# Performance work log

Hardware: AMD Instinct MI355X
Metric: run time of the kernel (lower is better)

## Reference

```python
import jax, jax.numpy as jnp
import numpy as np

SINKHORN_ITERS = 20
SINKHORN_TEMP = 0.2


def log_sinkhorn(log_alpha, n_iters=SINKHORN_ITERS, temperature=SINKHORN_TEMP):
    """Log-domain Sinkhorn normalization over the last two dims."""
    log_alpha = log_alpha / temperature
    for _ in range(n_iters):
        log_alpha = log_alpha - jax.nn.logsumexp(log_alpha, axis=-1, keepdims=True)
        log_alpha = log_alpha - jax.nn.logsumexp(log_alpha, axis=-2, keepdims=True)
    return jnp.exp(log_alpha)


def setup_inputs() -> dict:
    key = jax.random.key(0)
    k_x, k_a, k_w1, k_wv = jax.random.split(key, 4)
    B = 64
    N, K, BASIS = 1024, 64, 8
    # xavier-uniform-like init scales
    a_bound = np.sqrt(6.0 / (N + N))
    w1_bound = np.sqrt(6.0 / (N + BASIS))
    wv_bound = np.sqrt(6.0 / (K + K))
    x = jax.random.normal(k_x, (B, N * K), dtype=jnp.float32)
    A_logits = jax.random.uniform(k_a, (N, N), dtype=jnp.float32, minval=-a_bound, maxval=a_bound)
    W_1 = jax.random.uniform(k_w1, (N, BASIS), dtype=jnp.float32, minval=-w1_bound, maxval=w1_bound)
    W_V = jax.random.uniform(k_wv, (BASIS, K, K), dtype=jnp.float32, minval=-wv_bound, maxval=wv_bound)
    return {"x": x, "A_logits": A_logits, "W_1": W_1, "W_V": W_V}


def reference(x, A_logits, W_1, W_V):
    B = x.shape[0]
    N, K = A_logits.shape[0], W_V.shape[-1]
    # Doubly-stochastic global mixing matrix A: [N, N]
    A = log_sinkhorn(A_logits)
    # Local block logits via basis combination: [N, K, K]
    W_logits = jnp.einsum('tk,kde->tde', W_1, W_V)
    W = log_sinkhorn(W_logits)
    x_reshaped = x.reshape(B, N, K)
    x_local = jnp.einsum('bni,nio->bno', x_reshaped, W)   # per-block KxK mix
    x_global = jnp.einsum('mn,bno->bmo', A, x_local)       # NxN block mix
    return x_global.reshape(B, N * K)
```

## Files before the change

kernel.cpp:

```cpp
#include <hip/hip_runtime.h>
#include <hip/hip_bf16.h>


#define N_DIM 1024
#define INV_T 5.0f
#define NBAR 16

typedef __attribute__((ext_vector_type(8))) short short8;
typedef __attribute__((ext_vector_type(4))) float float4v;

__device__ __forceinline__ float wave_red_sum(float x) {
#define DPP_ADD(C)                                                            \
  {                                                                           \
    int _y = __builtin_amdgcn_update_dpp(0, __float_as_int(x), (C), 0xf, 0xf, \
                                         true);                               \
    x += __int_as_float(_y);                                                  \
  }
  DPP_ADD(0x111);
  DPP_ADD(0x112);
  DPP_ADD(0x114);
  DPP_ADD(0x118);
  DPP_ADD(0x142);
  DPP_ADD(0x143);
#undef DPP_ADD
  return x;
}

__global__ __launch_bounds__(1024) void k_front(
    const float* __restrict__ x, const float* __restrict__ L,
    const float* __restrict__ W1, const float* __restrict__ WV,
    float* __restrict__ E0, __hip_bfloat16* __restrict__ Eh,
    __hip_bfloat16* __restrict__ El, float* __restrict__ P,
    unsigned* __restrict__ ctrl, float* __restrict__ u_g,
    float* __restrict__ v_g, float* __restrict__ XL, int write_bf16) {
  __shared__ __align__(16) float smem[9600];
  const int t = threadIdx.x;
  const int bid = blockIdx.x;
  const int lane = t & 63;
  const int w = t >> 6;

  if (bid < NBAR) {
    float* v_s = smem;
    float* uS = smem + 1024;
    float* red = smem + 1024 + 64;
    const int b = bid;
    const int r0 = b * 64;
    unsigned* flags = ctrl;

    float e[4][16];
#pragma unroll
    for (int j = 0; j < 4; ++j) {
      const int r = r0 + 4 * w + j;
      const float4* Lr = (const float4*)(L + (size_t)r * N_DIM + lane * 16);
#pragma unroll
      for (int q = 0; q < 4; ++q) {
        float4 f = Lr[q];
        e[j][4 * q + 0] = __expf(f.x * INV_T);
        e[j][4 * q + 1] = __expf(f.y * INV_T);
        e[j][4 * q + 2] = __expf(f.z * INV_T);
        e[j][4 * q + 3] = __expf(f.w * INV_T);
      }
      const size_t off = (size_t)r * N_DIM + lane * 16;
      if (write_bf16) {
        __align__(16) ushort hb[16], lb[16];
#pragma unroll
        for (int q = 0; q < 16; ++q) {
          __hip_bfloat16 h = __float2bfloat16(e[j][q]);
          hb[q] = *(ushort*)&h;
          __hip_bfloat16 l2 = __float2bfloat16(e[j][q] - __bfloat162float(h));
          lb[q] = *(ushort*)&l2;
        }
        *(uint4*)&Eh[off] = *(uint4*)&hb[0];
        *(uint4*)&Eh[off + 8] = *(uint4*)&hb[8];
        *(uint4*)&El[off] = *(uint4*)&lb[0];
        *(uint4*)&El[off + 8] = *(uint4*)&lb[8];
      } else {
        float4* Er = (float4*)(E0 + off);
#pragma unroll
        for (int q = 0; q < 4; ++q) {
          float4 g;
          g.x = e[j][4 * q + 0];
          g.y = e[j][4 * q + 1];
          g.z = e[j][4 * q + 2];
          g.w = e[j][4 * q + 3];
          Er[q] = g;
        }
      }
    }
    v_s[t] = 1.0f;
    __syncthreads();

    float u[4];
    for (int it = 0; it < 20; ++it) {
      float vv[16];
#pragma unroll
      for (int q = 0; q < 4; ++q)
        *(float4*)&vv[4 * q] = *(const float4*)&v_s[lane * 16 + 4 * q];
#pragma unroll
      for (int j = 0; j < 4; ++j) {
        float p = 0.f;
#pragma unroll
        for (int k = 0; k < 16; ++k) p += e[j][k] * vv[k];
        p = wave_red_sum(p);
        float ps =
            __int_as_float(__builtin_amdgcn_readlane(__float_as_int(p), 63));
        u[j] = 1.0f / ps;
      }
      float cpl[16];
#pragma unroll
      for (int k = 0; k < 16; ++k)
        cpl[k] = e[0][k] * u[0] + e[1][k] * u[1] + e[2][k] * u[2] +
                 e[3][k] * u[3];
      if (w >= 8) {
#pragma unroll
        for (int q = 0; q < 4; ++q)
          *(float4*)&red[(w - 8) * 1032 + lane * 16 + 4 * q] =
              *(float4*)&cpl[4 * q];
      }
      __syncthreads();
      if (w < 8) {
        float* rr = &red[w * 1032 + lane * 16];
#pragma unroll
        for (int q = 0; q < 4; ++q) {
          float4 rv = *(float4*)&rr[4 * q];
          rv.x += cpl[4 * q + 0];
          rv.y += cpl[4 * q + 1];
          rv.z += cpl[4 * q + 2];
          rv.w += cpl[4 * q + 3];
          *(float4*)&rr[4 * q] = rv;
        }
      }
      __syncthreads();
      float cp = 0.f;
#pragma unroll
      for (int ww = 0; ww < 8; ++ww) cp += red[ww * 1032 + t];
      float* Pw = P + (it & 1) * (NBAR * N_DIM);
      __hip_atomic_store(&Pw[b * N_DIM + t], cp, __ATOMIC_RELAXED,
                         __HIP_MEMORY_SCOPE_AGENT);
      if (it == 19 && lane == 0) {
#pragma unroll
        for (int j = 0; j < 4; ++j) uS[4 * w + j] = u[j];
      }
      __syncthreads();
      if (t == 0)
        __hip_atomic_store(&flags[b], (unsigned)(it + 1), __ATOMIC_RELAXED,
                           __HIP_MEMORY_SCOPE_AGENT);
      if (w == 0 && lane < NBAR) {
        while (__hip_atomic_load(&flags[lane], __ATOMIC_RELAXED,
                                 __HIP_MEMORY_SCOPE_AGENT) <
               (unsigned)(it + 1))
          __builtin_amdgcn_s_sleep(2);
      }
      __syncthreads();
      float s2 = 0.f;
#pragma unroll
      for (int pb = 0; pb < NBAR; ++pb)
        s2 += __hip_atomic_load(&Pw[pb * N_DIM + t], __ATOMIC_RELAXED,
                                __HIP_MEMORY_SCOPE_AGENT);
      v_s[t] = 1.0f / s2;
      __syncthreads();
    }
    if (t < 64) u_g[r0 + t] = uS[t];
    if (b == 0) v_g[t] = v_s[t];
  } else {
    float* uS2 = smem;
    float* ps = smem + 64;
    float* Ws = smem + 64 + 1024;
    float* Xs = smem + 64 + 1024 + 4096;
    const int idx = bid - NBAR;
    const int cnt = (idx < 64) ? 5 : 4;
    const int base_n = (idx < 64) ? idx * 5 : 320 + (idx - 64) * 4;

    for (int s = 0; s < cnt; ++s) {
      const int n = base_n + s;
      float w1[8];
#pragma unroll
      for (int k = 0; k < 8; ++k) w1[k] = W1[n * 8 + k];

      float ew[4];
#pragma unroll
      for (int j = 0; j < 4; ++j) {
        const int f = j * 1024 + t;
        float acc = 0.f;
#pragma unroll
        for (int k = 0; k < 8; ++k) acc += w1[k] * WV[k * 4096 + f];
        ew[j] = __expf(acc * INV_T);
      }

      float vt = 1.0f;
      for (int it = 0; it < 20; ++it) {
#pragma unroll
        for (int j = 0; j < 4; ++j) {
          float pp = wave_red_sum(ew[j] * vt);
          if (lane == 63) uS2[j * 16 + w] = 1.0f / pp;
        }
        float cp = 0.f;
#pragma unroll
        for (int j = 0; j < 4; ++j) cp += ew[j] * uS2[j * 16 + w];
        ps[w * 64 + lane] = cp;
        __syncthreads();
        float sv = 0.f;
#pragma unroll
        for (int ww = 0; ww < 16; ++ww) sv += ps[ww * 64 + lane];
        vt = 1.0f / sv;
        __syncthreads();
      }

#pragma unroll
      for (int j = 0; j < 4; ++j)
        Ws[(j * 16 + w) * 64 + lane] = ew[j] * uS2[j * 16 + w] * vt;
#pragma unroll
      for (int j = 0; j < 4; ++j) {
        const int f = j * 1024 + t;
        Xs[(f >> 6) * 65 + (f & 63)] =
            x[(size_t)(f >> 6) * 65536 + n * 64 + (f & 63)];
      }
      __syncthreads();

      const int bb = t >> 4;
      const int o4 = (t & 15) * 4;
      float4 a4 = {0.f, 0.f, 0.f, 0.f};
#pragma unroll 4
      for (int i = 0; i < 64; ++i) {
        float4 w4 = *(const float4*)&Ws[i * 64 + o4];
        float xv = Xs[bb * 65 + i];
        a4.x += xv * w4.x;
        a4.y += xv * w4.y;
        a4.z += xv * w4.z;
        a4.w += xv * w4.w;
      }
      *(float4*)&XL[(size_t)n * 4096 + bb * 64 + o4] = a4;
      __syncthreads();
    }
  }
}

__global__ __launch_bounds__(256) void k_xt(const float* __restrict__ XL,
                                            const float* __restrict__ v_g,
                                            __hip_bfloat16* __restrict__ XTh,
                                            __hip_bfloat16* __restrict__ XTl) {
  __shared__ float T[64 * 68];
  __shared__ float vsh[64];
  const int t = threadIdx.x;
  const int n0 = blockIdx.x * 64;
  const int c0 = blockIdx.y * 64;
  if (t < 64) vsh[t] = v_g[n0 + t];
  {
    const int r = t >> 4;
    const int c4 = (t & 15) * 4;
#pragma unroll
    for (int p = 0; p < 4; ++p) {
      float4 f =
          *(const float4*)&XL[(size_t)(n0 + r + 16 * p) * 4096 + c0 + c4];
      *(float4*)&T[(r + 16 * p) * 68 + c4] = f;
    }
  }
  __syncthreads();
  const int cl = t >> 2;
  const int nb = (t & 3) * 16;
  __align__(16) __hip_bfloat16 hbuf[16];
  __align__(16) __hip_bfloat16 lbuf[16];
#pragma unroll
  for (int j = 0; j < 16; ++j) {
    float xv = T[(nb + j) * 68 + cl] * vsh[nb + j];
    __hip_bfloat16 h = __float2bfloat16(xv);
    hbuf[j] = h;
    lbuf[j] = __float2bfloat16(xv - __bfloat162float(h));
  }
  const size_t off = (size_t)(c0 + cl) * 1024 + n0 + nb;
  *(uint4*)&XTh[off] = *(uint4*)&hbuf[0];
  *(uint4*)&XTh[off + 8] = *(uint4*)&hbuf[8];
  *(uint4*)&XTl[off] = *(uint4*)&lbuf[0];
  *(uint4*)&XTl[off + 8] = *(uint4*)&lbuf[8];
}

#define LSTR 72
__global__ __launch_bounds__(256) void k_gemm3(
    const ushort* __restrict__ Eh, const ushort* __restrict__ El,
    const ushort* __restrict__ XTh, const ushort* __restrict__ XTl,
    const float* __restrict__ u_g, float* __restrict__ out) {
  __shared__ ushort As[128 * LSTR];
  __shared__ ushort Xs[128 * LSTR];
  __shared__ float ush[128];
  const int t = threadIdx.x;
  const int m0 = blockIdx.x * 128;
  const int c0 = blockIdx.y * 128;
  const int wid = t >> 6, lane = t & 63;
  const int wm = (wid & 1) * 64, wc = (wid >> 1) * 64;
  const int lm = lane & 15, q = lane >> 4;
  const int sr = t >> 1;
  const int sc = (t & 1) * 32;
  if (t < 128) ush[t] = u_g[m0 + t];

  float4v acc[4][4];
#pragma unroll
  for (int i = 0; i < 4; ++i)
#pragma unroll
    for (int j = 0; j < 4; ++j) acc[i][j] = (float4v){0.f, 0.f, 0.f, 0.f};

  for (int seg = 0; seg < 3; ++seg) {
    const ushort* Ag = (seg == 1) ? El : Eh;
    const ushort* Xg = (seg == 2) ? XTl : XTh;
    for (int k0 = 0; k0 < 1024; k0 += 64) {
      __syncthreads();
      const ushort* ag = Ag + (size_t)(m0 + sr) * 1024 + k0 + sc;
      const ushort* xg = Xg + (size_t)(c0 + sr) * 1024 + k0 + sc;
      uint4 a0 = *(const uint4*)(ag);
      uint4 a1 = *(const uint4*)(ag + 8);
      uint4 a2 = *(const uint4*)(ag + 16);
      uint4 a3 = *(const uint4*)(ag + 24);
      uint4 x0 = *(const uint4*)(xg);
      uint4 x1 = *(const uint4*)(xg + 8);
      uint4 x2 = *(const uint4*)(xg + 16);
      uint4 x3 = *(const uint4*)(xg + 24);
      *(uint4*)&As[sr * LSTR + sc] = a0;
      *(uint4*)&As[sr * LSTR + sc + 8] = a1;
      *(uint4*)&As[sr * LSTR + sc + 16] = a2;
      *(uint4*)&As[sr * LSTR + sc + 24] = a3;
      *(uint4*)&Xs[sr * LSTR + sc] = x0;
      *(uint4*)&Xs[sr * LSTR + sc + 8] = x1;
      *(uint4*)&Xs[sr * LSTR + sc + 16] = x2;
      *(uint4*)&Xs[sr * LSTR + sc + 24] = x3;
      __syncthreads();
#pragma unroll
      for (int kk = 0; kk < 2; ++kk) {
        short8 af[4], xf[4];
#pragma unroll
        for (int i = 0; i < 4; ++i)
          af[i] = *(const short8*)&As[(wm + 16 * i + lm) * LSTR + kk * 32 +
                                      q * 8];
#pragma unroll
        for (int j = 0; j < 4; ++j)
          xf[j] = *(const short8*)&Xs[(wc + 16 * j + lm) * LSTR + kk * 32 +
                                      q * 8];
#pragma unroll
        for (int i = 0; i < 4; ++i)
#pragma unroll
          for (int j = 0; j < 4; ++j)
            acc[i][j] = __builtin_amdgcn_mfma_f32_16x16x32_bf16(
                af[i], xf[j], acc[i][j], 0, 0, 0);
      }
    }
  }
#pragma unroll
  for (int i = 0; i < 4; ++i) {
#pragma unroll
    for (int j = 0; j < 4; ++j) {
      const int ml = wm + 16 * i + q * 4;
      const int m = m0 + ml;
      const int c = c0 + wc + 16 * j + lm;
      const int bb = c >> 6, o = c & 63;
      float* dst = out + (size_t)bb * 65536 + (size_t)m * 64 + o;
#pragma unroll
      for (int r = 0; r < 4; ++r) dst[64 * r] = acc[i][j][r] * ush[ml + r];
    }
  }
}

__global__ __launch_bounds__(256) void k_gemm(const float* __restrict__ E0,
                                              const float* __restrict__ XL,
                                              const float* __restrict__ u_g,
                                              const float* __restrict__ v_g,
                                              float* __restrict__ out) {
  __shared__ float Asm[32][132];
  __shared__ float Xsm[32][132];
  const int t = threadIdx.x;
  const int m0 = blockIdx.x * 128;
  const int c0 = blockIdx.y * 128;
  const int my8 = (t >> 4) * 8;
  const int cx8 = (t & 15) * 8;
  const int kk = t & 31;
  const int rr = t >> 5;
  float acc[8][8] = {};

  for (int k0 = 0; k0 < 1024; k0 += 32) {
#pragma unroll
    for (int s = 0; s < 16; ++s)
      Asm[kk][rr + 8 * s] = E0[(size_t)(m0 + rr + 8 * s) * 1024 + k0 + kk];
#pragma unroll
    for (int s = 0; s < 4; ++s) {
      const int krow = k0 + rr + 8 * s;
      float vk = v_g[krow];
      float4 f = *(const float4*)&XL[(size_t)krow * 4096 + c0 + kk * 4];
      f.x *= vk;
      f.y *= vk;
      f.z *= vk;
      f.w *= vk;
      *(float4*)&Xsm[rr + 8 * s][kk * 4] = f;
    }
    __syncthreads();
#pragma unroll
    for (int k = 0; k < 32; ++k) {
      float a[8], xv[8];
      *(float4*)&a[0] = *(const float4*)&Asm[k][my8];
      *(float4*)&a[4] = *(const float4*)&Asm[k][my8 + 4];
      *(float4*)&xv[0] = *(const float4*)&Xsm[k][cx8];
      *(float4*)&xv[4] = *(const float4*)&Xsm[k][cx8 + 4];
#pragma unroll
      for (int i = 0; i < 8; ++i)
#pragma unroll
        for (int j = 0; j < 8; ++j) acc[i][j] += a[i] * xv[j];
    }
    __syncthreads();
  }

#pragma unroll
  for (int i = 0; i < 8; ++i) {
    const int m = m0 + my8 + i;
    const float um = u_g[m];
    const int c = c0 + cx8;
    const int bb = c >> 6, o = c & 63;
    float* dst = out + (size_t)bb * 65536 + (size_t)m * 64 + o;
#pragma unroll
    for (int j = 0; j < 8; ++j) dst[j] = acc[i][j] * um;
  }
}

extern "C" void kernel_launch(void* const* d_in, const int* in_sizes, int n_in,
                              void* d_out, int out_size, void* d_ws,
                              size_t ws_size, hipStream_t stream) {
  (void)in_sizes;
  (void)n_in;
  (void)out_size;
  const float* x = (const float*)d_in[0];
  const float* Alog = (const float*)d_in[1];
  const float* W1 = (const float*)d_in[2];
  const float* WV = (const float*)d_in[3];
  float* out = (float*)d_out;

  char* ws = (char*)d_ws;
  const size_t MB = 1024 * 1024;
  const size_t KB = 1024;
  const bool use_bf16 = ws_size >= (40 * MB + 256 * KB);

  float* E0;
  float* XL;
  float* P;
  float* u_g;
  float* v_g;
  unsigned* ctrl;
  __hip_bfloat16 *Eh = nullptr, *El = nullptr, *XTh = nullptr, *XTl = nullptr;
  if (use_bf16) {
    E0 = (float*)(ws);
    XL = (float*)(ws + 4 * MB);
    Eh = (__hip_bfloat16*)(ws + 20 * MB);
    El = (__hip_bfloat16*)(ws + 22 * MB);
    XTh = (__hip_bfloat16*)(ws + 24 * MB);
    XTl = (__hip_bfloat16*)(ws + 32 * MB);
    P = (float*)(ws + 40 * MB);
    u_g = (float*)(ws + 40 * MB + 128 * KB);
    v_g = (float*)(ws + 40 * MB + 132 * KB);
    ctrl = (unsigned*)(ws + 40 * MB + 136 * KB);
  } else {
    E0 = (float*)(ws);
    XL = (float*)(ws + 4 * MB);
    P = (float*)(ws + 20 * MB);
    u_g = (float*)(ws + 20 * MB + 128 * KB);
    v_g = (float*)(ws + 20 * MB + 132 * KB);
    ctrl = (unsigned*)(ws + 20 * MB + 136 * KB);
  }

  hipMemsetAsync(ctrl, 0, 4096, stream);
  hipLaunchKernelGGL(k_front, dim3(256), dim3(1024), 0, stream, x, Alog, W1,
                     WV, E0, Eh, El, P, ctrl, u_g, v_g, XL, use_bf16 ? 1 : 0);
  if (use_bf16) {
    hipLaunchKernelGGL(k_xt, dim3(16, 64), dim3(256), 0, stream, XL, v_g, XTh,
                       XTl);
    hipLaunchKernelGGL(k_gemm3, dim3(8, 32), dim3(256), 0, stream,
                       (const ushort*)Eh, (const ushort*)El, (const ushort*)XTh,
                       (const ushort*)XTl, u_g, out);
  } else {
    hipLaunchKernelGGL(k_gemm, dim3(8, 32), dim3(256), 0, stream, E0, XL, u_g,
                       v_g, out);
  }
}
```

Before: 275.9 us.

## Replace flag barrier with sentinel polling and add dynamic work queue

The Sinkhorn blocks no longer use a per-iteration flag barrier. Each iteration writes its partial column sums into its own zeroed slice of P, and readers poll those values directly until none is zero. The slices are cleared by an added memset. After finishing the A-Sinkhorn, those blocks join the per-block W work through an atomic ticket queue, replacing the static assignment, to balance load. The element layout of E and of the reduction buffer changes from per-lane contiguous to lane-interleaved. The trade-offs are an extra memset launch, narrower bf16 stores, and reliance on a zero sentinel that assumes no partial sum is exactly zero.

```diff
diff --git a/kernel.cpp b/kernel.cpp
--- a/kernel.cpp
+++ b/kernel.cpp
@@ -45,66 +45,45 @@
     float* red = smem + 1024 + 64;
     const int b = bid;
     const int r0 = b * 64;
-    unsigned* flags = ctrl;
 
     float e[4][16];
 #pragma unroll
     for (int j = 0; j < 4; ++j) {
       const int r = r0 + 4 * w + j;
-      const float4* Lr = (const float4*)(L + (size_t)r * N_DIM + lane * 16);
-#pragma unroll
-      for (int q = 0; q < 4; ++q) {
-        float4 f = Lr[q];
-        e[j][4 * q + 0] = __expf(f.x * INV_T);
-        e[j][4 * q + 1] = __expf(f.y * INV_T);
-        e[j][4 * q + 2] = __expf(f.z * INV_T);
-        e[j][4 * q + 3] = __expf(f.w * INV_T);
-      }
-      const size_t off = (size_t)r * N_DIM + lane * 16;
+      const float* Lr = L + (size_t)r * N_DIM + lane;
+#pragma unroll
+      for (int k = 0; k < 16; ++k) e[j][k] = __expf(Lr[k * 64] * INV_T);
       if (write_bf16) {
-        __align__(16) ushort hb[16], lb[16];
-#pragma unroll
-        for (int q = 0; q < 16; ++q) {
-          __hip_bfloat16 h = __float2bfloat16(e[j][q]);
-          hb[q] = *(ushort*)&h;
-          __hip_bfloat16 l2 = __float2bfloat16(e[j][q] - __bfloat162float(h));
-          lb[q] = *(ushort*)&l2;
+        __hip_bfloat16* EhR = Eh + (size_t)r * N_DIM + lane;
+        __hip_bfloat16* ElR = El + (size_t)r * N_DIM + lane;
+#pragma unroll
+        for (int k = 0; k < 16; ++k) {
+          __hip_bfloat16 h = __float2bfloat16(e[j][k]);
+          EhR[k * 64] = h;
+          ElR[k * 64] = __float2bfloat16(e[j][k] - __bfloat162float(h));
         }
-        *(uint4*)&Eh[off] = *(uint4*)&hb[0];
-        *(uint4*)&Eh[off + 8] = *(uint4*)&hb[8];
-        *(uint4*)&El[off] = *(uint4*)&lb[0];
-        *(uint4*)&El[off + 8] = *(uint4*)&lb[8];
       } else {
-        float4* Er = (float4*)(E0 + off);
-#pragma unroll
-        for (int q = 0; q < 4; ++q) {
-          float4 g;
-          g.x = e[j][4 * q + 0];
-          g.y = e[j][4 * q + 1];
-          g.z = e[j][4 * q + 2];
-          g.w = e[j][4 * q + 3];
-          Er[q] = g;
-        }
+        float* ER = E0 + (size_t)r * N_DIM + lane;
+#pragma unroll
+        for (int k = 0; k < 16; ++k) ER[k * 64] = e[j][k];
       }
     }
     v_s[t] = 1.0f;
     __syncthreads();
 
-    float u[4];
     for (int it = 0; it < 20; ++it) {
       float vv[16];
 #pragma unroll
-      for (int q = 0; q < 4; ++q)
-        *(float4*)&vv[4 * q] = *(const float4*)&v_s[lane * 16 + 4 * q];
+      for (int k = 0; k < 16; ++k) vv[k] = v_s[k * 64 + lane];
+      float u[4];
 #pragma unroll
       for (int j = 0; j < 4; ++j) {
         float p = 0.f;
 #pragma unroll
         for (int k = 0; k < 16; ++k) p += e[j][k] * vv[k];
         p = wave_red_sum(p);
-        float ps =
-            __int_as_float(__builtin_amdgcn_readlane(__float_as_int(p), 63));
-        u[j] = 1.0f / ps;
+        u[j] = 1.0f /
+               __int_as_float(__builtin_amdgcn_readlane(__float_as_int(p), 63));
       }
       float cpl[16];
 #pragma unroll
@@ -113,66 +92,75 @@
                  e[3][k] * u[3];
       if (w >= 8) {
 #pragma unroll
-        for (int q = 0; q < 4; ++q)
-          *(float4*)&red[(w - 8) * 1032 + lane * 16 + 4 * q] =
-              *(float4*)&cpl[4 * q];
+        for (int k = 0; k < 16; ++k)
+          red[(w - 8) * 1028 + k * 64 + lane] = cpl[k];
       }
       __syncthreads();
       if (w < 8) {
-        float* rr = &red[w * 1032 + lane * 16];
-#pragma unroll
-        for (int q = 0; q < 4; ++q) {
-          float4 rv = *(float4*)&rr[4 * q];
-          rv.x += cpl[4 * q + 0];
-          rv.y += cpl[4 * q + 1];
-          rv.z += cpl[4 * q + 2];
-          rv.w += cpl[4 * q + 3];
-          *(float4*)&rr[4 * q] = rv;
-        }
+#pragma unroll
+        for (int k = 0; k < 16; ++k) red[w * 1028 + k * 64 + lane] += cpl[k];
       }
       __syncthreads();
       float cp = 0.f;
 #pragma unroll
-      for (int ww = 0; ww < 8; ++ww) cp += red[ww * 1032 + t];
-      float* Pw = P + (it & 1) * (NBAR * N_DIM);
-      __hip_atomic_store(&Pw[b * N_DIM + t], cp, __ATOMIC_RELAXED,
+      for (int ww = 0; ww < 8; ++ww) cp += red[ww * 1028 + t];
+      float* Pit = P + (size_t)it * (NBAR * N_DIM);
+      __hip_atomic_store(&Pit[b * N_DIM + t], cp, __ATOMIC_RELAXED,
                          __HIP_MEMORY_SCOPE_AGENT);
       if (it == 19 && lane == 0) {
 #pragma unroll
         for (int j = 0; j < 4; ++j) uS[4 * w + j] = u[j];
       }
-      __syncthreads();
-      if (t == 0)
-        __hip_atomic_store(&flags[b], (unsigned)(it + 1), __ATOMIC_RELAXED,
-                           __HIP_MEMORY_SCOPE_AGENT);
-      if (w == 0 && lane < NBAR) {
-        while (__hip_atomic_load(&flags[lane], __ATOMIC_RELAXED,
-                                 __HIP_MEMORY_SCOPE_AGENT) <
-               (unsigned)(it + 1))
-          __builtin_amdgcn_s_sleep(2);
-      }
-      __syncthreads();
+      unsigned vals[NBAR];
+#pragma unroll
+      for (int pb = 0; pb < NBAR; ++pb)
+        vals[pb] = (pb == b)
+                       ? __float_as_uint(cp)
+                       : __hip_atomic_load(
+                             (const unsigned*)&Pit[pb * N_DIM + t],
+                             __ATOMIC_RELAXED, __HIP_MEMORY_SCOPE_AGENT);
+      for (;;) {
+        unsigned miss = 0u;
+#pragma unroll
+        for (int pb = 0; pb < NBAR; ++pb) miss |= (vals[pb] == 0u) ? 1u : 0u;
+        if (miss == 0u) break;
+#pragma unroll
+        for (int pb = 0; pb < NBAR; ++pb)
+          if (vals[pb] == 0u)
+            vals[pb] = __hip_atomic_load(
+                (const unsigned*)&Pit[pb * N_DIM + t], __ATOMIC_RELAXED,
+                __HIP_MEMORY_SCOPE_AGENT);
+      }
       float s2 = 0.f;
 #pragma unroll
-      for (int pb = 0; pb < NBAR; ++pb)
-        s2 += __hip_atomic_load(&Pw[pb * N_DIM + t], __ATOMIC_RELAXED,
-                                __HIP_MEMORY_SCOPE_AGENT);
+      for (int pb = 0; pb < NBAR; ++pb) s2 += __uint_as_float(vals[pb]);
       v_s[t] = 1.0f / s2;
       __syncthreads();
     }
     if (t < 64) u_g[r0 + t] = uS[t];
     if (b == 0) v_g[t] = v_s[t];
-  } else {
+    __syncthreads();
+  }
+
+  {
     float* uS2 = smem;
     float* ps = smem + 64;
     float* Ws = smem + 64 + 1024;
     float* Xs = smem + 64 + 1024 + 4096;
-    const int idx = bid - NBAR;
-    const int cnt = (idx < 64) ? 5 : 4;
-    const int base_n = (idx < 64) ? idx * 5 : 320 + (idx - 64) * 4;
-
-    for (int s = 0; s < cnt; ++s) {
-      const int n = base_n + s;
+    unsigned* nsh = (unsigned*)(smem + 9500);
+    unsigned* ticket = ctrl + 64;
+
+    if (t == 0)
+      nsh[0] = __hip_atomic_fetch_add(ticket, 1u, __ATOMIC_RELAXED,
+                                      __HIP_MEMORY_SCOPE_AGENT);
+    __syncthreads();
+    int slot = 0;
+    for (;;) {
+      const unsigned n = nsh[slot];
+      if (n >= 1024u) break;
+      if (t == 0)
+        nsh[slot ^ 1] = __hip_atomic_fetch_add(ticket, 1u, __ATOMIC_RELAXED,
+                                               __HIP_MEMORY_SCOPE_AGENT);
       float w1[8];
 #pragma unroll
       for (int k = 0; k < 8; ++k) w1[k] = W1[n * 8 + k];
@@ -194,10 +182,10 @@
           float pp = wave_red_sum(ew[j] * vt);
           if (lane == 63) uS2[j * 16 + w] = 1.0f / pp;
         }
-        float cp = 0.f;
-#pragma unroll
-        for (int j = 0; j < 4; ++j) cp += ew[j] * uS2[j * 16 + w];
-        ps[w * 64 + lane] = cp;
+        float cp2 = 0.f;
+#pragma unroll
+        for (int j = 0; j < 4; ++j) cp2 += ew[j] * uS2[j * 16 + w];
+        ps[w * 64 + lane] = cp2;
         __syncthreads();
         float sv = 0.f;
 #pragma unroll
@@ -231,6 +219,7 @@
       }
       *(float4*)&XL[(size_t)n * 4096 + bb * 64 + o4] = a4;
       __syncthreads();
+      slot ^= 1;
     }
   }
 }
@@ -432,6 +421,7 @@
   const size_t MB = 1024 * 1024;
   const size_t KB = 1024;
   const bool use_bf16 = ws_size >= (40 * MB + 256 * KB);
+  const size_t P_BYTES = 20ull * NBAR * N_DIM * sizeof(float);
 
   float* E0;
   float* XL;
@@ -441,26 +431,27 @@
   unsigned* ctrl;
   __hip_bfloat16 *Eh = nullptr, *El = nullptr, *XTh = nullptr, *XTl = nullptr;
   if (use_bf16) {
+    P = (float*)(ws);
     E0 = (float*)(ws);
     XL = (float*)(ws + 4 * MB);
     Eh = (__hip_bfloat16*)(ws + 20 * MB);
     El = (__hip_bfloat16*)(ws + 22 * MB);
     XTh = (__hip_bfloat16*)(ws + 24 * MB);
     XTl = (__hip_bfloat16*)(ws + 32 * MB);
-    P = (float*)(ws + 40 * MB);
-    u_g = (float*)(ws + 40 * MB + 128 * KB);
-    v_g = (float*)(ws + 40 * MB + 132 * KB);
-    ctrl = (unsigned*)(ws + 40 * MB + 136 * KB);
+    u_g = (float*)(ws + 40 * MB);
+    v_g = (float*)(ws + 40 * MB + 4 * KB);
+    ctrl = (unsigned*)(ws + 40 * MB + 8 * KB);
   } else {
     E0 = (float*)(ws);
     XL = (float*)(ws + 4 * MB);
     P = (float*)(ws + 20 * MB);
-    u_g = (float*)(ws + 20 * MB + 128 * KB);
-    v_g = (float*)(ws + 20 * MB + 132 * KB);
-    ctrl = (unsigned*)(ws + 20 * MB + 136 * KB);
+    u_g = (float*)(ws + 20 * MB + 1536 * KB);
+    v_g = (float*)(ws + 20 * MB + 1540 * KB);
+    ctrl = (unsigned*)(ws + 20 * MB + 1544 * KB);
   }
 
   hipMemsetAsync(ctrl, 0, 4096, stream);
+  hipMemsetAsync(P, 0, P_BYTES, stream);
   hipLaunchKernelGGL(k_front, dim3(256), dim3(1024), 0, stream, x, Alog, W1,
                      WV, E0, Eh, El, P, ctrl, u_g, v_g, XL, use_bf16 ? 1 : 0);
   if (use_bf16) {
```

Measured after the change: 282.1 us. +2.3%, slower.
